# Kernel optimization log

Measured on AMD Instinct MI355X. Metric: run time of the kernel, lower is better.

## Reference

```python
import jax, jax.numpy as jnp
import numpy as np

TOP_K = 30
NUM_RBF = 16
NUM_POS = 16
MAX_REL = 32
EDGE_FEATURES = 128
EDGE_IN = NUM_POS + NUM_RBF * 9 + 7  # 167


def _normalize(x, axis=-1):
    # torch F.normalize: x / max(||x||, 1e-12)
    return x / jnp.maximum(jnp.linalg.norm(x, axis=axis, keepdims=True), 1e-12)


def _gather_nodes(nodes, idx):
    # nodes [B,L,C], idx [B,L,K] -> [B,L,K,C]
    return jax.vmap(lambda n, i: n[i])(nodes, idx)


def _rbf(D):
    D_mu = jnp.linspace(2.0, 22.0, NUM_RBF)  # [R]
    D_sigma = (22.0 - 2.0) / NUM_RBF
    return jnp.exp(-(((D[..., None] - D_mu) / D_sigma) ** 2))


def _get_rbf(A, B, E_idx):
    # full pairwise dist then gather neighbors (faithful to source)
    D_A_B = jnp.sqrt(jnp.sum((A[:, :, None, :] - B[:, None, :, :]) ** 2, -1) + 1e-6)
    D_nb = jnp.take_along_axis(D_A_B, E_idx, axis=2)  # [B,L,K]
    return _rbf(D_nb)


def _quaternions(R):
    # R [B,L,K,3,3] -> Q [B,L,K,4]
    diag = jnp.diagonal(R, axis1=-2, axis2=-1)  # [B,L,K,3]
    Rxx, Ryy, Rzz = diag[..., 0], diag[..., 1], diag[..., 2]
    magnitudes = 0.5 * jnp.sqrt(jnp.abs(1 + jnp.stack(
        [Rxx - Ryy - Rzz, -Rxx + Ryy - Rzz, -Rxx - Ryy + Rzz], -1)))
    signs = jnp.sign(jnp.stack([
        R[..., 2, 1] - R[..., 1, 2],
        R[..., 0, 2] - R[..., 2, 0],
        R[..., 1, 0] - R[..., 0, 1]], -1))
    xyz = signs * magnitudes
    w = jnp.sqrt(jax.nn.relu(1 + jnp.sum(diag, -1, keepdims=True))) / 2.0
    return _normalize(jnp.concatenate((xyz, w), -1))


def _orientations_coarse(X, E_idx, eps=1e-6):
    B, L, _ = X.shape
    dX = X[:, 1:, :] - X[:, :-1, :]
    dX_norm = jnp.linalg.norm(dX, axis=-1)
    dX_mask = (dX_norm > 3.6) & (dX_norm < 4.0)
    dX = dX * dX_mask[:, :, None]
    U = _normalize(dX)
    u_2, u_1, u_0 = U[:, :-2, :], U[:, 1:-1, :], U[:, 2:, :]
    n_2 = _normalize(jnp.cross(u_2, u_1))
    o_1 = _normalize(u_2 - u_1)
    # local frames O [B,L-3,3,3] -> flattened, padded to [B,L,9]
    O = jnp.stack((o_1, n_2, jnp.cross(o_1, n_2)), 2).reshape(B, L - 3, 9)
    O = jnp.pad(O, ((0, 0), (1, 2), (0, 0)))
    O_neighbors = _gather_nodes(O, E_idx)        # [B,L,K,9]
    X_neighbors = _gather_nodes(X, E_idx)        # [B,L,K,3]
    O = O.reshape(B, L, 3, 3)
    O_neighbors = O_neighbors.reshape(*E_idx.shape, 3, 3)
    dXn = X_neighbors - X[:, :, None, :]
    dU = _normalize(jnp.einsum('blij,blkj->blki', O, dXn))
    R = jnp.einsum('blji,blkjm->blkim', O, O_neighbors)  # O^T @ O_nb
    Q = _quaternions(R)
    return jnp.concatenate((dU, Q), -1)  # [B,L,K,7]


def setup_inputs() -> dict:
    B, L = 2, 4096
    key = jax.random.key(0)
    ks = jax.random.split(key, 6)
    Ca = jax.random.normal(ks[0], (B, L, 3), dtype=jnp.float32)
    mask = jnp.ones((B, L), dtype=jnp.float32)
    residue_idx = jnp.arange(B * L, dtype=jnp.int32).reshape(B, L)
    chain_labels = jnp.sort(jax.random.randint(ks[1], (B, L), 0, 4), axis=-1).astype(jnp.int32)
    pos_in = 2 * MAX_REL + 1 + 1  # 66
    pos_W = jax.random.normal(ks[2], (NUM_POS, pos_in), dtype=jnp.float32) / np.sqrt(pos_in)
    pos_b = jnp.zeros((NUM_POS,), dtype=jnp.float32)
    edge_W = jax.random.normal(ks[3], (EDGE_FEATURES, EDGE_IN), dtype=jnp.float32) / np.sqrt(EDGE_IN)
    ln_g = jnp.ones((EDGE_FEATURES,), dtype=jnp.float32)
    ln_b = jnp.zeros((EDGE_FEATURES,), dtype=jnp.float32)
    return {"Ca": Ca, "mask": mask, "residue_idx": residue_idx,
            "chain_labels": chain_labels, "pos_W": pos_W, "pos_b": pos_b,
            "edge_W": edge_W, "ln_g": ln_g, "ln_b": ln_b}


def _forward(Ca, mask, residue_idx, chain_labels, pos_W, pos_b, edge_W, ln_g, ln_b):
    B, L, _ = Ca.shape
    # _dist: masked pairwise distances + kNN
    mask_2D = mask[:, :, None] * mask[:, None, :]
    dX = Ca[:, None, :, :] - Ca[:, :, None, :]
    D = mask_2D * jnp.sqrt(jnp.sum(dX ** 2, 3) + 1e-6)
    D_max = jnp.max(D, -1, keepdims=True)
    D_adjust = D + (1.0 - mask_2D) * D_max
    k = min(TOP_K, L)
    neg_vals, E_idx = jax.lax.top_k(-D_adjust, k)  # smallest-k
    D_neighbors = -neg_vals

    zeros = jnp.zeros((B, 1, 3), dtype=Ca.dtype)
    Ca_0 = jnp.concatenate([zeros, Ca[:, :-1, :]], axis=1)
    Ca_1 = Ca
    Ca_2 = jnp.concatenate([Ca[:, 1:, :], zeros], axis=1)

    O_features = _orientations_coarse(Ca, E_idx)

    RBF_all = jnp.concatenate([
        _rbf(D_neighbors),
        _get_rbf(Ca_0, Ca_0, E_idx), _get_rbf(Ca_2, Ca_2, E_idx),
        _get_rbf(Ca_0, Ca_1, E_idx), _get_rbf(Ca_0, Ca_2, E_idx),
        _get_rbf(Ca_1, Ca_0, E_idx), _get_rbf(Ca_1, Ca_2, E_idx),
        _get_rbf(Ca_2, Ca_0, E_idx), _get_rbf(Ca_2, Ca_1, E_idx)], axis=-1)

    offset = residue_idx[:, :, None] - residue_idx[:, None, :]
    offset = jnp.take_along_axis(offset, E_idx, axis=2)  # [B,L,K]
    d_chains = (chain_labels[:, :, None] - chain_labels[:, None, :] == 0).astype(jnp.int32)
    E_chains = jnp.take_along_axis(d_chains, E_idx, axis=2)

    # PositionalEncodings
    d = jnp.clip(offset + MAX_REL, 0, 2 * MAX_REL) * E_chains + (1 - E_chains) * (2 * MAX_REL + 1)
    d_onehot = jax.nn.one_hot(d, 2 * MAX_REL + 2, dtype=jnp.float32)
    E_positional = d_onehot @ pos_W.T + pos_b

    E = jnp.concatenate((E_positional, RBF_all, O_features), -1)  # [B,L,K,167]
    E = E @ edge_W.T
    mu = jnp.mean(E, -1, keepdims=True)
    var = jnp.var(E, -1, keepdims=True)
    E = (E - mu) / jnp.sqrt(var + 1e-5) * ln_g + ln_b
    return E, E_idx


def reference(Ca, mask, residue_idx, chain_labels, pos_W, pos_b, edge_W, ln_g, ln_b):
    return _forward(Ca, mask, residue_idx, chain_labels, pos_W, pos_b, edge_W, ln_g, ln_b)
```

## Files before the change

kernel.cpp:

```cpp
#include <hip/hip_runtime.h>
#include <stdint.h>

#define LL 4096
#define NB 2
#define KK 30
#define CDIM 128
#define FROW 200

typedef _Float16 half_t;
typedef half_t half8 __attribute__((ext_vector_type(8)));
typedef float f32x4 __attribute__((ext_vector_type(4)));

__device__ __forceinline__ float3 loadCa(const float* __restrict__ Ca, int b, int idx) {
    const float* p = Ca + ((size_t)(b * LL + idx)) * 3;
    return make_float3(p[0], p[1], p[2]);
}
__device__ __forceinline__ float3 shiftedCa(const float* __restrict__ Ca, int b, int idx, int sel) {
    int jj = idx + sel - 1;
    if (jj < 0 || jj >= LL) return make_float3(0.f, 0.f, 0.f);
    return loadCa(Ca, b, jj);
}
__device__ __forceinline__ float sgnf(float x) { return (x > 0.f) ? 1.f : ((x < 0.f) ? -1.f : 0.f); }
__device__ __forceinline__ float pdist(float3 a, float3 c) {
    float dx = a.x - c.x, dy = a.y - c.y, dz = a.z - c.z;
    return sqrtf(dx * dx + dy * dy + dz * dz + 1e-6f);
}

__global__ __launch_bounds__(256) void prep_kernel(const float* __restrict__ W,
                                                   const float* __restrict__ posW,
                                                   const float* __restrict__ posb,
                                                   const float* __restrict__ Ca,
                                                   half_t* __restrict__ Bp,
                                                   half_t* __restrict__ pwt,
                                                   float* __restrict__ Of) {
    int blk = blockIdx.x;
    int tid = threadIdx.x;
    if (blk < 12) {
        int idx = blk * 256 + tid;
        if (idx >= 8 * 6 * 64) return;
        int l = idx & 63;
        int ts = idx >> 6;
        int s = ts % 6, t = ts / 6;
        int n = 16 * t + (l & 15);
        int kbase = 32 * s + 8 * (l >> 4);
        half8 v;
#pragma unroll
        for (int e = 0; e < 8; e++) {
            int k = kbase + e;
            v[e] = (k < 167) ? (half_t)W[n * 167 + k] : (half_t)0.f;
        }
        *(half8*)(Bp + (size_t)idx * 8) = v;
    } else if (blk < 17) {
        int idx = (blk - 12) * 256 + tid;
        if (idx < 66 * 16) {
            int d = idx >> 4, p = idx & 15;
            pwt[d * 16 + p] = (half_t)(posW[p * 66 + d] + posb[p]);
        }
    } else {
        int t = (blk - 17) * 256 + tid;
        if (t >= NB * LL) return;
        int b = t >> 12, i = t & (LL - 1);
        float o[9] = {0.f, 0.f, 0.f, 0.f, 0.f, 0.f, 0.f, 0.f, 0.f};
        if (i >= 1 && i <= LL - 3) {
            float3 cm = loadCa(Ca, b, i - 1), cc = loadCa(Ca, b, i), cp = loadCa(Ca, b, i + 1);
            float dx0 = cc.x - cm.x, dy0 = cc.y - cm.y, dz0 = cc.z - cm.z;
            float n0 = sqrtf(dx0 * dx0 + dy0 * dy0 + dz0 * dz0);
            float k0 = (n0 > 3.6f && n0 < 4.0f) ? 1.f : 0.f;
            float s0 = k0 / fmaxf(n0 * k0, 1e-12f);
            float u2x = dx0 * s0, u2y = dy0 * s0, u2z = dz0 * s0;
            float dx1 = cp.x - cc.x, dy1 = cp.y - cc.y, dz1 = cp.z - cc.z;
            float n1 = sqrtf(dx1 * dx1 + dy1 * dy1 + dz1 * dz1);
            float k1 = (n1 > 3.6f && n1 < 4.0f) ? 1.f : 0.f;
            float s1 = k1 / fmaxf(n1 * k1, 1e-12f);
            float u1x = dx1 * s1, u1y = dy1 * s1, u1z = dz1 * s1;
            float cx = u2y * u1z - u2z * u1y;
            float cy = u2z * u1x - u2x * u1z;
            float cz = u2x * u1y - u2y * u1x;
            float cn = sqrtf(cx * cx + cy * cy + cz * cz);
            float cinv = 1.f / fmaxf(cn, 1e-12f);
            float n2x = cx * cinv, n2y = cy * cinv, n2z = cz * cinv;
            float ox = u2x - u1x, oy = u2y - u1y, oz = u2z - u1z;
            float on = sqrtf(ox * ox + oy * oy + oz * oz);
            float oinv = 1.f / fmaxf(on, 1e-12f);
            float o1x = ox * oinv, o1y = oy * oinv, o1z = oz * oinv;
            o[0] = o1x; o[1] = o1y; o[2] = o1z;
            o[3] = n2x; o[4] = n2y; o[5] = n2z;
            o[6] = o1y * n2z - o1z * n2y;
            o[7] = o1z * n2x - o1x * n2z;
            o[8] = o1x * n2y - o1y * n2x;
        }
        float* dst = Of + (size_t)t * 9;
#pragma unroll
        for (int r = 0; r < 9; r++) dst[r] = o[r];
    }
}

__global__ __launch_bounds__(256, 8) void topk_kernel(const float* __restrict__ Ca,
                                                      const float* __restrict__ mask,
                                                      int* __restrict__ eidx_ws,
                                                      float* __restrict__ dnb_ws,
                                                      float* __restrict__ out_eidx_f) {
    __shared__ unsigned long long cand[512];
    __shared__ int wint[2][4];
    __shared__ int gcnt[4];
    __shared__ float wflt[4];
    int row = blockIdx.x;
    int b = row >> 12;
    int tid = threadIdx.x;
    int w = tid >> 6, lane = tid & 63;
    float3 ci = loadCa(Ca, b, row & (LL - 1));
    float mi = mask[row];
    float dreg[16];
    float localmax = 0.f;
#pragma unroll
    for (int s = 0; s < 16; s++) {
        int j = tid + s * 256;
        const float* pj = Ca + ((size_t)(b * LL + j)) * 3;
        float dx = pj[0] - ci.x, dy = pj[1] - ci.y, dz = pj[2] - ci.z;
        float d = sqrtf(dx * dx + dy * dy + dz * dz + 1e-6f);
        float D = mi * mask[b * LL + j] * d;
        dreg[s] = D;
        localmax = fmaxf(localmax, D);
    }
#pragma unroll
    for (int o = 32; o; o >>= 1) localmax = fmaxf(localmax, __shfl_xor(localmax, o));
    if (lane == 0) wflt[w] = localmax;
    __syncthreads();
    float dmax = fmaxf(fmaxf(wflt[0], wflt[1]), fmaxf(wflt[2], wflt[3]));
    unsigned ui[16];
#pragma unroll
    for (int s = 0; s < 16; s++) {
        int j = tid + s * 256;
        float m2 = mi * mask[b * LL + j];
        ui[s] = __float_as_uint(dreg[s] + (1.0f - m2) * dmax);
    }
    unsigned lo = 0u, hi = 0x7f800000u, T = 0u;
    bool found = false;
    int p = 0;
    for (int it = 0; it < 24 && !found; ++it) {
        unsigned mid = (lo + hi) >> 1;
        int c = 0;
#pragma unroll
        for (int s = 0; s < 16; s++) c += (ui[s] < mid) ? 1 : 0;
#pragma unroll
        for (int o = 32; o; o >>= 1) c += __shfl_xor(c, o);
        if (lane == 0) wint[p][w] = c;
        __syncthreads();
        c = wint[p][0] + wint[p][1] + wint[p][2] + wint[p][3];
        p ^= 1;
        if (c < 30) lo = mid;
        else if (c > 64) hi = mid;
        else { T = mid; found = true; }
    }
    if (!found) T = hi;
    int cnt = 0;
#pragma unroll
    for (int s = 0; s < 16; s++) cnt += (ui[s] < T) ? 1 : 0;
    int inc = cnt;
#pragma unroll
    for (int o = 1; o < 64; o <<= 1) {
        int nv = __shfl_up(inc, o);
        if (lane >= o) inc += nv;
    }
    if (lane == 63) gcnt[w] = inc;
    __syncthreads();
    int C = gcnt[0] + gcnt[1] + gcnt[2] + gcnt[3];
    int waveoff = 0;
    for (int q = 0; q < 4; q++) waveoff += (q < w) ? gcnt[q] : 0;
    int slot = waveoff + inc - cnt;
#pragma unroll
    for (int s = 0; s < 16; s++) {
        if (ui[s] < T) {
            int j = tid + s * 256;
            if (slot < 512)
                cand[slot] = ((unsigned long long)ui[s] << 32) | (unsigned)j;
            slot++;
        }
    }
    __syncthreads();
    if (w != 0) return;
    if (C <= 64) {
        unsigned long long v = (lane < C) ? cand[lane] : ~0ull;
#pragma unroll
        for (int k = 2; k <= 64; k <<= 1) {
#pragma unroll
            for (int jj = k >> 1; jj > 0; jj >>= 1) {
                unsigned long long o = __shfl_xor(v, jj);
                bool take_min = (((lane & jj) == 0) == ((lane & k) == 0));
                bool lt = (o < v);
                v = (take_min == lt) ? o : v;
            }
        }
        if (lane < KK) {
            int j = (int)(v & 0xffffffffu);
            eidx_ws[row * KK + lane] = j;
            dnb_ws[row * KK + lane] = __uint_as_float((unsigned)(v >> 32));
            out_eidx_f[row * KK + lane] = (float)j;
        }
    } else {
        unsigned long long r[8];
#pragma unroll
        for (int q = 0; q < 8; q++) {
            int idx = lane + 64 * q;
            r[q] = (idx < C && idx < 512) ? cand[idx] : ~0ull;
        }
        for (int t = 0; t < KK; t++) {
            unsigned long long v = r[0];
#pragma unroll
            for (int q = 1; q < 8; q++) v = (r[q] < v) ? r[q] : v;
#pragma unroll
            for (int o = 32; o; o >>= 1) {
                unsigned long long u = __shfl_xor(v, o);
                if (u < v) v = u;
            }
            if (lane == 0) {
                int j = (int)(v & 0xffffffffu);
                eidx_ws[row * KK + t] = j;
                dnb_ws[row * KK + t] = __uint_as_float((unsigned)(v >> 32));
                out_eidx_f[row * KK + t] = (float)j;
            }
#pragma unroll
            for (int q = 0; q < 8; q++)
                if (r[q] == v) r[q] = ~0ull;
        }
    }
}

__global__ __launch_bounds__(256) void edge_kernel(const float* __restrict__ Ca,
                                                   const int* __restrict__ ridx,
                                                   const int* __restrict__ chl,
                                                   const half_t* __restrict__ pwt,
                                                   const half_t* __restrict__ Bp,
                                                   const float* __restrict__ ln_g,
                                                   const float* __restrict__ ln_b,
                                                   const float* __restrict__ Of,
                                                   const int* __restrict__ eidx_ws,
                                                   const float* __restrict__ dnb_ws,
                                                   float* __restrict__ outE) {
    __shared__ alignas(16) half_t featH[64][FROW];
    __shared__ float sD[60][10];
    int row0 = blockIdx.x * 2;
    int b = row0 >> 12;
    int tid = threadIdx.x;

    if (tid < 120) {
        int e = tid >> 1, half = tid & 1;
        int isr1 = (e >= KK) ? 1 : 0;
        int grow = row0 + isr1;
        int ke = e - (isr1 ? KK : 0);
        int i = grow & (LL - 1);
        int j = eidx_ws[grow * KK + ke];
        if (half == 0) {
            float3 Pi0 = shiftedCa(Ca, b, i, 0);
            float3 Pi2 = shiftedCa(Ca, b, i, 2);
            float3 Pj0 = shiftedCa(Ca, b, j, 0);
            float3 Pj1 = loadCa(Ca, b, j);
            float3 Pj2 = shiftedCa(Ca, b, j, 2);
            sD[e][0] = dnb_ws[grow * KK + ke];
            sD[e][1] = pdist(Pi0, Pj0);
            sD[e][2] = pdist(Pi2, Pj2);
            sD[e][3] = pdist(Pi0, Pj1);
            sD[e][4] = pdist(Pi0, Pj2);
            int off = ridx[grow] - ridx[b * LL + j];
            int eqc = (chl[grow] == chl[b * LL + j]) ? 1 : 0;
            int d = off + 32;
            d = d < 0 ? 0 : (d > 64 ? 64 : d);
            d = eqc ? d : 65;
            *(half8*)&featH[e][0] = *(const half8*)(pwt + d * 16);
            *(half8*)&featH[e][8] = *(const half8*)(pwt + d * 16 + 8);
        } else {
            float3 Pi1 = loadCa(Ca, b, i);
            float3 Pi2 = shiftedCa(Ca, b, i, 2);
            float3 Pj0 = shiftedCa(Ca, b, j, 0);
            float3 Pj1 = loadCa(Ca, b, j);
            float3 Pj2 = shiftedCa(Ca, b, j, 2);
            sD[e][5] = pdist(Pi1, Pj0);
            sD[e][6] = pdist(Pi1, Pj2);
            sD[e][7] = pdist(Pi2, Pj0);
            sD[e][8] = pdist(Pi2, Pj1);
            float Oi[9], Oj[9];
#pragma unroll
            for (int r = 0; r < 9; r++) {
                Oi[r] = Of[(size_t)grow * 9 + r];
                Oj[r] = Of[((size_t)(b * LL + j)) * 9 + r];
            }
            float dx = Pj1.x - Pi1.x, dy = Pj1.y - Pi1.y, dz = Pj1.z - Pi1.z;
            float v0 = Oi[0] * dx + Oi[1] * dy + Oi[2] * dz;
            float v1 = Oi[3] * dx + Oi[4] * dy + Oi[5] * dz;
            float v2 = Oi[6] * dx + Oi[7] * dy + Oi[8] * dz;
            float nn = sqrtf(v0 * v0 + v1 * v1 + v2 * v2);
            float ninv = 1.f / fmaxf(nn, 1e-12f);
            float R[3][3];
#pragma unroll
            for (int m = 0; m < 3; m++)
#pragma unroll
                for (int n = 0; n < 3; n++)
                    R[m][n] = Oi[0 * 3 + m] * Oj[0 * 3 + n] + Oi[1 * 3 + m] * Oj[1 * 3 + n] +
                              Oi[2 * 3 + m] * Oj[2 * 3 + n];
            float Rxx = R[0][0], Ryy = R[1][1], Rzz = R[2][2];
            float m0 = 0.5f * sqrtf(fabsf(1.f + Rxx - Ryy - Rzz));
            float m1 = 0.5f * sqrtf(fabsf(1.f - Rxx + Ryy - Rzz));
            float m2 = 0.5f * sqrtf(fabsf(1.f - Rxx - Ryy + Rzz));
            float x = sgnf(R[2][1] - R[1][2]) * m0;
            float y = sgnf(R[0][2] - R[2][0]) * m1;
            float z = sgnf(R[1][0] - R[0][1]) * m2;
            float ww = 0.5f * sqrtf(fmaxf(1.f + Rxx + Ryy + Rzz, 0.f));
            float qn = sqrtf(x * x + y * y + z * z + ww * ww);
            float qi = 1.f / fmaxf(qn, 1e-12f);
            half8 h;
            h[0] = (half_t)(v0 * ninv);
            h[1] = (half_t)(v1 * ninv);
            h[2] = (half_t)(v2 * ninv);
            h[3] = (half_t)(x * qi);
            h[4] = (half_t)(y * qi);
            h[5] = (half_t)(z * qi);
            h[6] = (half_t)(ww * qi);
            h[7] = (half_t)0.f;
            half8 zv = {};
            *(half8*)&featH[e][160] = h;
            *(half8*)&featH[e][168] = zv;
            *(half8*)&featH[e][176] = zv;
            *(half8*)&featH[e][184] = zv;
        }
    } else if (tid >= 156) {
        int t = tid - 156;
        int r = 60 + t / 25, c = t % 25;
        half8 zv = {};
        *(half8*)&featH[r][c * 8] = zv;
    }
    __syncthreads();

    for (int job = tid; job < 540; job += 256) {
        int e = job / 9, q = job - e * 9;
        float D = sD[e][q];
        half8 v0, v1;
#pragma unroll
        for (int m = 0; m < 8; m++) {
            float mu = 2.0f + (4.f / 3.f) * (float)m;
            float t = (D - mu) * 0.8f;
            v0[m] = (half_t)exp2f(t * t * -1.4426950408889634f);
        }
#pragma unroll
        for (int m = 8; m < 16; m++) {
            float mu = 2.0f + (4.f / 3.f) * (float)m;
            float t = (D - mu) * 0.8f;
            v1[m - 8] = (half_t)exp2f(t * t * -1.4426950408889634f);
        }
        *(half8*)&featH[e][16 + 16 * q] = v0;
        *(half8*)&featH[e][24 + 16 * q] = v1;
    }
    __syncthreads();

    int lane = tid & 63, w = tid >> 6;
    int col = lane & 15, g = lane >> 4;
    half8 af[6];
#pragma unroll
    for (int s = 0; s < 6; s++)
        af[s] = *(const half8*)&featH[16 * w + col][32 * s + 8 * g];
    f32x4 zero = {0.f, 0.f, 0.f, 0.f};
    f32x4 acc[8];
#pragma unroll
    for (int t = 0; t < 8; t++) acc[t] = zero;
#pragma unroll
    for (int t = 0; t < 8; t++) {
#pragma unroll
        for (int s = 0; s < 6; s++) {
            half8 bf = *(const half8*)(Bp + ((size_t)((t * 6 + s) * 64 + lane)) * 8);
            acc[t] = __builtin_amdgcn_mfma_f32_16x16x32_f16(af[s], bf, acc[t], 0, 0, 0);
        }
    }
    float mu[4], invs[4];
#pragma unroll
    for (int q = 0; q < 4; q++) {
        float s = 0.f;
#pragma unroll
        for (int t = 0; t < 8; t++) s += acc[t][q];
#pragma unroll
        for (int o = 1; o < 16; o <<= 1) s += __shfl_xor(s, o);
        mu[q] = s * (1.f / 128.f);
    }
#pragma unroll
    for (int q = 0; q < 4; q++) {
        float vs = 0.f;
#pragma unroll
        for (int t = 0; t < 8; t++) {
            float d = acc[t][q] - mu[q];
            vs += d * d;
        }
#pragma unroll
        for (int o = 1; o < 16; o <<= 1) vs += __shfl_xor(vs, o);
        invs[q] = 1.f / sqrtf(vs * (1.f / 128.f) + 1e-5f);
    }
    float lgv[8], lbv[8];
#pragma unroll
    for (int t = 0; t < 8; t++) {
        lgv[t] = ln_g[16 * t + col];
        lbv[t] = ln_b[16 * t + col];
    }
#pragma unroll
    for (int q = 0; q < 4; q++) {
        int eq = 16 * w + 4 * g + q;
        if (eq < 60) {
            int grow = row0 + (eq >= KK ? 1 : 0);
            int ke = eq - (eq >= KK ? KK : 0);
            float* dst = outE + ((size_t)(grow * KK + ke)) * CDIM + col;
#pragma unroll
            for (int t = 0; t < 8; t++)
                dst[16 * t] = (acc[t][q] - mu[q]) * invs[q] * lgv[t] + lbv[t];
        }
    }
}

extern "C" void kernel_launch(void* const* d_in, const int* in_sizes, int n_in,
                              void* d_out, int out_size, void* d_ws, size_t ws_size,
                              hipStream_t stream) {
    const float* Ca = (const float*)d_in[0];
    const float* mask = (const float*)d_in[1];
    const int* ridx = (const int*)d_in[2];
    const int* chl = (const int*)d_in[3];
    const float* posW = (const float*)d_in[4];
    const float* posb = (const float*)d_in[5];
    const float* edgeW = (const float*)d_in[6];
    const float* lng = (const float*)d_in[7];
    const float* lnb = (const float*)d_in[8];

    float* outE = (float*)d_out;
    float* outEidxF = outE + (size_t)NB * LL * KK * CDIM;

    char* ws = (char*)d_ws;
    half_t* Bp = (half_t*)ws;
    half_t* pwt = (half_t*)(ws + 49152);
    float* Of = (float*)(ws + 51264);
    int* eidx = (int*)(ws + 346176);
    float* dnb = (float*)(ws + 1329216);

    prep_kernel<<<17 + (NB * LL + 255) / 256, 256, 0, stream>>>(edgeW, posW, posb, Ca, Bp, pwt, Of);
    topk_kernel<<<NB * LL, 256, 0, stream>>>(Ca, mask, eidx, dnb, outEidxF);
    edge_kernel<<<NB * LL / 2, 256, 0, stream>>>(Ca, ridx, chl, pwt, Bp, lng, lnb,
                                                 Of, eidx, dnb, outE);
}
```

Before: 117.9 us.

## Split GEMM by output columns per wave and reduce LayerNorm stats through shared memory

Each wave now computes all 64 edge rows for its own 32 output columns instead of 16 rows across all 128 columns. Each wave therefore loads only a quarter of the packed weight matrix (12 fragments instead of 48), which cuts global/L2 weight traffic, at the cost of more LDS reads of the feature tile. LayerNorm statistics become a one-pass sum and sum-of-squares, combined across waves via shared memory with two extra barriers. The one-pass variance formula is slightly less numerically robust, and it is clamped at zero.

```diff
diff --git a/kernel.cpp b/kernel.cpp
--- a/kernel.cpp
+++ b/kernel.cpp
@@ -239,6 +239,9 @@
                                                    float* __restrict__ outE) {
     __shared__ alignas(16) half_t featH[64][FROW];
     __shared__ float sD[60][10];
+    __shared__ float psum[64][4];
+    __shared__ float pssq[64][4];
+    __shared__ float rmu[64], rinv[64];
     int row0 = blockIdx.x * 2;
     int b = row0 >> 12;
     int tid = threadIdx.x;
@@ -352,61 +355,83 @@
     __syncthreads();
 
     int lane = tid & 63, w = tid >> 6;
-    int col = lane & 15, g = lane >> 4;
-    half8 af[6];
-#pragma unroll
-    for (int s = 0; s < 6; s++)
-        af[s] = *(const half8*)&featH[16 * w + col][32 * s + 8 * g];
+    int cc = lane & 15, g = lane >> 4;
     f32x4 zero = {0.f, 0.f, 0.f, 0.f};
-    f32x4 acc[8];
-#pragma unroll
-    for (int t = 0; t < 8; t++) acc[t] = zero;
-#pragma unroll
-    for (int t = 0; t < 8; t++) {
-#pragma unroll
-        for (int s = 0; s < 6; s++) {
-            half8 bf = *(const half8*)(Bp + ((size_t)((t * 6 + s) * 64 + lane)) * 8);
-            acc[t] = __builtin_amdgcn_mfma_f32_16x16x32_f16(af[s], bf, acc[t], 0, 0, 0);
-        }
-    }
-    float mu[4], invs[4];
-#pragma unroll
-    for (int q = 0; q < 4; q++) {
-        float s = 0.f;
-#pragma unroll
-        for (int t = 0; t < 8; t++) s += acc[t][q];
-#pragma unroll
-        for (int o = 1; o < 16; o <<= 1) s += __shfl_xor(s, o);
-        mu[q] = s * (1.f / 128.f);
-    }
-#pragma unroll
-    for (int q = 0; q < 4; q++) {
-        float vs = 0.f;
-#pragma unroll
-        for (int t = 0; t < 8; t++) {
-            float d = acc[t][q] - mu[q];
-            vs += d * d;
-        }
-#pragma unroll
-        for (int o = 1; o < 16; o <<= 1) vs += __shfl_xor(vs, o);
-        invs[q] = 1.f / sqrtf(vs * (1.f / 128.f) + 1e-5f);
-    }
-    float lgv[8], lbv[8];
-#pragma unroll
-    for (int t = 0; t < 8; t++) {
-        lgv[t] = ln_g[16 * t + col];
-        lbv[t] = ln_b[16 * t + col];
-    }
-#pragma unroll
-    for (int q = 0; q < 4; q++) {
-        int eq = 16 * w + 4 * g + q;
-        if (eq < 60) {
-            int grow = row0 + (eq >= KK ? 1 : 0);
-            int ke = eq - (eq >= KK ? KK : 0);
-            float* dst = outE + ((size_t)(grow * KK + ke)) * CDIM + col;
-#pragma unroll
-            for (int t = 0; t < 8; t++)
-                dst[16 * t] = (acc[t][q] - mu[q]) * invs[q] * lgv[t] + lbv[t];
+    f32x4 acc[4][2];
+#pragma unroll
+    for (int m = 0; m < 4; m++) {
+        acc[m][0] = zero;
+        acc[m][1] = zero;
+    }
+    const half_t* b0p = Bp + ((size_t)(2 * w) * 6) * 64 * 8;
+    const half_t* b1p = Bp + ((size_t)(2 * w + 1) * 6) * 64 * 8;
+    for (int s = 0; s < 6; s++) {
+        int ko = 32 * s + 8 * g;
+        half8 af0 = *(const half8*)&featH[cc][ko];
+        half8 af1 = *(const half8*)&featH[16 + cc][ko];
+        half8 af2 = *(const half8*)&featH[32 + cc][ko];
+        half8 af3 = *(const half8*)&featH[48 + cc][ko];
+        half8 bf0 = *(const half8*)(b0p + (size_t)(s * 64 + lane) * 8);
+        half8 bf1 = *(const half8*)(b1p + (size_t)(s * 64 + lane) * 8);
+        acc[0][0] = __builtin_amdgcn_mfma_f32_16x16x32_f16(af0, bf0, acc[0][0], 0, 0, 0);
+        acc[0][1] = __builtin_amdgcn_mfma_f32_16x16x32_f16(af0, bf1, acc[0][1], 0, 0, 0);
+        acc[1][0] = __builtin_amdgcn_mfma_f32_16x16x32_f16(af1, bf0, acc[1][0], 0, 0, 0);
+        acc[1][1] = __builtin_amdgcn_mfma_f32_16x16x32_f16(af1, bf1, acc[1][1], 0, 0, 0);
+        acc[2][0] = __builtin_amdgcn_mfma_f32_16x16x32_f16(af2, bf0, acc[2][0], 0, 0, 0);
+        acc[2][1] = __builtin_amdgcn_mfma_f32_16x16x32_f16(af2, bf1, acc[2][1], 0, 0, 0);
+        acc[3][0] = __builtin_amdgcn_mfma_f32_16x16x32_f16(af3, bf0, acc[3][0], 0, 0, 0);
+        acc[3][1] = __builtin_amdgcn_mfma_f32_16x16x32_f16(af3, bf1, acc[3][1], 0, 0, 0);
+    }
+
+#pragma unroll
+    for (int m = 0; m < 4; m++) {
+#pragma unroll
+        for (int q = 0; q < 4; q++) {
+            float v0 = acc[m][0][q], v1 = acc[m][1][q];
+            float sp = v0 + v1;
+            float qp = v0 * v0 + v1 * v1;
+#pragma unroll
+            for (int o = 1; o < 16; o <<= 1) {
+                sp += __shfl_xor(sp, o);
+                qp += __shfl_xor(qp, o);
+            }
+            if (cc == 0) {
+                int r = 16 * m + 4 * g + q;
+                psum[r][w] = sp;
+                pssq[r][w] = qp;
+            }
+        }
+    }
+    __syncthreads();
+    if (tid < 64) {
+        float sum = psum[tid][0] + psum[tid][1] + psum[tid][2] + psum[tid][3];
+        float ssq = pssq[tid][0] + pssq[tid][1] + pssq[tid][2] + pssq[tid][3];
+        float mu = sum * (1.f / 128.f);
+        float var = fmaxf(ssq * (1.f / 128.f) - mu * mu, 0.f);
+        rmu[tid] = mu;
+        rinv[tid] = 1.f / sqrtf(var + 1e-5f);
+    }
+    __syncthreads();
+
+    float lgv[2], lbv[2];
+#pragma unroll
+    for (int tt = 0; tt < 2; tt++) {
+        lgv[tt] = ln_g[32 * w + 16 * tt + cc];
+        lbv[tt] = ln_b[32 * w + 16 * tt + cc];
+    }
+#pragma unroll
+    for (int m = 0; m < 4; m++) {
+#pragma unroll
+        for (int q = 0; q < 4; q++) {
+            int r = 16 * m + 4 * g + q;
+            if (r < 60) {
+                float mu = rmu[r], invs = rinv[r];
+                int grow = row0 + (r >= KK ? 1 : 0);
+                int ke = r - (r >= KK ? KK : 0);
+                float* dst = outE + ((size_t)(grow * KK + ke)) * CDIM + 32 * w + cc;
+                dst[0] = (acc[m][0][q] - mu) * invs * lgv[0] + lbv[0];
+                dst[16] = (acc[m][1][q] - mu) * invs * lgv[1] + lbv[1];
+            }
         }
     }
 }
```

After: 116.3 us. About the same (-1.4%).
